# Optimization experiments

Hardware: AMD Instinct MI355X
Metric: run time of the kernel (lower is better)

## Reference

```python
import jax, jax.numpy as jnp
import numpy as np

# Asymmetric NF4 lookup table: NFQuantizer.create_normal_map(offset=0.9677083, num_bits=4)
NF4_TABLE = jnp.array([
    -1.0, -0.6961928009986877, -0.5250730514526367, -0.39491748809814453,
    -0.28444138169288635, -0.18477343022823334, -0.09105003625154495, 0.0,
    0.07958029955625534, 0.16093020141124725, 0.24611230194568634,
    0.33791524171829224, 0.44070982933044434, 0.5626170039176941,
    0.7229568362236023, 1.0], dtype=jnp.float32)

OUT_FEATURES = 4096
IN_FEATURES = 4096
BLOCK_SIZE = 64
NUM_BITS = 4

def setup_inputs() -> dict:
    key = jax.random.key(0)
    k1, k2, k3, k4, k5 = jax.random.split(key, 5)
    n_packed = OUT_FEATURES * IN_FEATURES // (8 // NUM_BITS)      # 8388608
    n_blocks = OUT_FEATURES * IN_FEATURES // BLOCK_SIZE            # 262144
    return {
        "input": jax.random.normal(k1, (2, 1024, IN_FEATURES), dtype=jnp.float32),
        "qweight": jax.random.randint(k2, (n_packed, 1), 0, 256, dtype=jnp.int32),
        "absmax": jax.random.uniform(k3, (n_blocks, 1), dtype=jnp.float32, minval=0.01, maxval=0.05),
        "lora_A": jax.random.normal(k4, (64, IN_FEATURES), dtype=jnp.float32) * 0.02,
        "lora_B": jax.random.normal(k5, (OUT_FEATURES, 64), dtype=jnp.float32) * 0.02,
    }

def dequantize_block(qweight, absmax):
    q = qweight[:, 0]                         # [N/2] packed bytes (int)
    low = NF4_TABLE[q & 0xF]                  # sub-code i=0 (low nibble first)
    high = NF4_TABLE[(q >> 4) & 0xF]          # sub-code i=1
    w = jnp.stack([low, high], axis=-1)       # [N/2, 2], matches torch column order
    w = w.reshape(-1, BLOCK_SIZE) * absmax    # per-block rescale, absmax [n_blocks,1]
    return w.reshape(OUT_FEATURES, IN_FEATURES)

def reference(input, qweight, absmax, lora_A, lora_B):
    weight = dequantize_block(qweight, absmax)          # [out, in] fp32
    ret = input @ weight.T                              # [B, S, out]
    lora = (input @ lora_A.T) @ lora_B.T                # low-rank path
    return ret + lora
```

## Files before the change

kernel.cpp:

```cpp
#include <hip/hip_runtime.h>
#include <hip/hip_bf16.h>
#include <stdint.h>

#define M_DIM 2048
#define N_DIM 4096
#define K_DIM 4096

typedef __attribute__((ext_vector_type(8))) __bf16 bf16x8;
typedef __attribute__((ext_vector_type(4))) float f32x4;
typedef __attribute__((ext_vector_type(8))) unsigned short u16x8;

__device__ __constant__ float NF4_TAB[16] = {
    -1.0f, -0.6961928009986877f, -0.5250730514526367f, -0.39491748809814453f,
    -0.28444138169288635f, -0.18477343022823334f, -0.09105003625154495f, 0.0f,
    0.07958029955625534f, 0.16093020141124725f, 0.24611230194568634f,
    0.33791524171829224f, 0.44070982933044434f, 0.5626170039176941f,
    0.7229568362236023f, 1.0f};

__device__ inline unsigned short f2b(float f) {
  union { float f; uint32_t u; } v; v.f = f;
  uint32_t u = v.u;
  return (unsigned short)((u + 0x7fffu + ((u >> 16) & 1u)) >> 16);
}

__global__ void k_cvt(const float4* __restrict__ in, ushort4* __restrict__ out, int n) {
  int i = blockIdx.x * 256 + threadIdx.x;
  if (i < n) {
    float4 v = in[i];
    ushort4 o;
    o.x = f2b(v.x); o.y = f2b(v.y); o.z = f2b(v.z); o.w = f2b(v.w);
    out[i] = o;
  }
}

__global__ void __launch_bounds__(256) k_build_w(const int* __restrict__ qw,
                                                 const float* __restrict__ am,
                                                 unsigned short* __restrict__ W) {
  __shared__ float tab[16];
  const int t = threadIdx.x;
  if (t < 16) tab[t] = NF4_TAB[t];
  __syncthreads();
  size_t i = (size_t)blockIdx.x * 256 + t;
  int4 q = *(const int4*)(qw + i * 4);
  float amv = am[i >> 3];
  u16x8 o;
  o[0] = f2b(tab[q.x & 15] * amv);  o[1] = f2b(tab[(q.x >> 4) & 15] * amv);
  o[2] = f2b(tab[q.y & 15] * amv);  o[3] = f2b(tab[(q.y >> 4) & 15] * amv);
  o[4] = f2b(tab[q.z & 15] * amv);  o[5] = f2b(tab[(q.z >> 4) & 15] * amv);
  o[6] = f2b(tab[q.w & 15] * amv);  o[7] = f2b(tab[(q.w >> 4) & 15] * amv);
  *(u16x8*)(W + i * 8) = o;
}

__global__ void __launch_bounds__(256) k_lora_u(const unsigned short* __restrict__ A16,
                                                const unsigned short* __restrict__ lA16,
                                                float* __restrict__ Up) {
  const int ln = threadIdx.x & 63, w = threadIdx.x >> 6;
  const int lr = ln & 15, lk = ln >> 4;
  const int mslab = blockIdx.x & 15;
  const int kc = blockIdx.x >> 4;
  const int m0 = mslab * 128 + w * 32;
  const int k0 = kc * 256;
  f32x4 acc[2][4] = {};
#pragma unroll
  for (int kk = 0; kk < 256; kk += 32) {
    bf16x8 af[2], bv[4];
#pragma unroll
    for (int mi = 0; mi < 2; ++mi)
      af[mi] = *(const bf16x8*)(A16 + (size_t)(m0 + mi * 16 + lr) * K_DIM + k0 + kk + lk * 8);
#pragma unroll
    for (int ni = 0; ni < 4; ++ni)
      bv[ni] = *(const bf16x8*)(lA16 + (size_t)(ni * 16 + lr) * K_DIM + k0 + kk + lk * 8);
#pragma unroll
    for (int mi = 0; mi < 2; ++mi)
#pragma unroll
      for (int ni = 0; ni < 4; ++ni)
        acc[mi][ni] = __builtin_amdgcn_mfma_f32_16x16x32_bf16(af[mi], bv[ni],
                                                              acc[mi][ni], 0, 0, 0);
  }
  float* up = Up + (size_t)kc * (M_DIM * 64);
#pragma unroll
  for (int mi = 0; mi < 2; ++mi)
#pragma unroll
    for (int ni = 0; ni < 4; ++ni)
#pragma unroll
      for (int r = 0; r < 4; ++r)
        up[(size_t)(m0 + mi * 16 + lk * 4 + r) * 64 + ni * 16 + lr] = acc[mi][ni][r];
}

__global__ void k_lora_red(const float4* __restrict__ Up, ushort4* __restrict__ U16) {
  int i = blockIdx.x * 256 + threadIdx.x;
  float4 s = Up[i];
#pragma unroll
  for (int c = 1; c < 16; ++c) {
    float4 p = Up[(size_t)c * (M_DIM * 64 / 4) + i];
    s.x += p.x; s.y += p.y; s.z += p.z; s.w += p.w;
  }
  ushort4 o; o.x = f2b(s.x); o.y = f2b(s.y); o.z = f2b(s.z); o.w = f2b(s.w);
  U16[i] = o;
}

#define LDSBUF 24576

#define FENCE() asm volatile("" ::: "memory")
#define BAR() do { FENCE(); __builtin_amdgcn_s_barrier(); FENCE(); } while (0)

#define COMPUTE_PHASE(KS, BC)                                                    \
  do {                                                                           \
    bf16x8 af[4], bv[4];                                                         \
    _Pragma("unroll") for (int mi = 0; mi < 4; ++mi) {                           \
      int row = wr * 64 + mi * 16 + lr;                                          \
      int slot = (((KS) << 2) | lk) ^ (row & 7);                                 \
      af[mi] = *(const bf16x8*)((BC) + row * 64 + slot * 8);                     \
    }                                                                            \
    _Pragma("unroll") for (int ni = 0; ni < 4; ++ni) {                           \
      int row = wc * 64 + ni * 16 + lr;                                          \
      int slot = (((KS) << 2) | lk) ^ (row & 7);                                 \
      bv[ni] = *(const bf16x8*)((BC) + 8192 + row * 64 + slot * 8);              \
    }                                                                            \
    __builtin_amdgcn_s_setprio(1);                                               \
    _Pragma("unroll") for (int mi = 0; mi < 4; ++mi)                             \
    _Pragma("unroll") for (int ni = 0; ni < 4; ++ni)                             \
      acc[mi][ni] = __builtin_amdgcn_mfma_f32_16x16x32_bf16(                     \
          af[mi], bv[ni], acc[mi][ni], 0, 0, 0);                                 \
    __builtin_amdgcn_s_setprio(0);                                               \
  } while (0)

__global__ void __launch_bounds__(512, 2) k_gemm(const unsigned short* __restrict__ A,
                                                 const unsigned short* __restrict__ B,
                                                 const unsigned short* __restrict__ U,
                                                 const unsigned short* __restrict__ LB,
                                                 float* __restrict__ C) {
  __shared__ unsigned short lds[3 * LDSBUF];
  const int tid = threadIdx.x;
  const int ln = tid & 63;
  const int wid = tid >> 6;
  const int wr = wid >> 2;
  const int wc = wid & 3;
  const int lr = ln & 15;
  const int lk = ln >> 4;

  const int sw = (blockIdx.x & 7) * 32 + (blockIdx.x >> 3);
  const int bm = sw & 15;
  const int bn = sw >> 4;
  const size_t arow0 = (size_t)bm * 128;
  const size_t brow0 = (size_t)bn * 256;

  const int srow = (wid << 3) + (ln >> 3);
  const int gs0 = (ln & 7) ^ (srow & 7);
  auto stage = [&](const unsigned short* __restrict__ G, size_t stride, size_t grow0,
                   int kt, unsigned short* dst) {
    const char* g = (const char*)(G + (grow0 + srow) * stride) + kt * 128 + gs0 * 16;
    __builtin_amdgcn_global_load_lds(
        (const __attribute__((address_space(1))) uint32_t*)g,
        (__attribute__((address_space(3))) uint32_t*)(dst + (size_t)(wid << 3) * 64),
        16, 0, 0);
  };

  f32x4 acc[4][4] = {};

  stage(A, K_DIM, arow0, 0, lds);
  stage(A, K_DIM, arow0 + 64, 0, lds + 4096);
  stage(B, K_DIM, brow0, 0, lds + 8192);
  stage(B, K_DIM, brow0 + 64, 0, lds + 12288);
  stage(B, K_DIM, brow0 + 128, 0, lds + 16384);
  stage(B, K_DIM, brow0 + 192, 0, lds + 20480);
  {
    unsigned short* b1 = lds + LDSBUF;
    stage(A, K_DIM, arow0, 1, b1);
    stage(A, K_DIM, arow0 + 64, 1, b1 + 4096);
    stage(B, K_DIM, brow0, 1, b1 + 8192);
    stage(B, K_DIM, brow0 + 64, 1, b1 + 12288);
    stage(B, K_DIM, brow0 + 128, 1, b1 + 16384);
    stage(B, K_DIM, brow0 + 192, 1, b1 + 20480);
  }
  asm volatile("s_waitcnt vmcnt(6)" ::: "memory");
  BAR();

  int cb = 0, sb = 2;
#pragma unroll 1
  for (int t = 0; t < 65; ++t) {
    const unsigned short* bc = lds + cb * LDSBUF;
    unsigned short* sd = lds + sb * LDSBUF;
    int kt2 = t + 2;
    const bool lora = (kt2 >= 64);
    const unsigned short* GA = lora ? U : A;
    const unsigned short* GB = lora ? LB : B;
    const size_t str = lora ? 64 : (size_t)K_DIM;
    const int ktv = lora ? 0 : kt2;

    stage(GA, str, arow0, ktv, sd);
    stage(GA, str, arow0 + 64, ktv, sd + 4096);
    stage(GB, str, brow0, ktv, sd + 8192);
    COMPUTE_PHASE(0, bc);
    BAR();

    stage(GB, str, brow0 + 64, ktv, sd + 12288);
    stage(GB, str, brow0 + 128, ktv, sd + 16384);
    stage(GB, str, brow0 + 192, ktv, sd + 20480);
    COMPUTE_PHASE(1, bc);
    asm volatile("s_waitcnt vmcnt(6)" ::: "memory");
    BAR();

    cb = (cb == 2) ? 0 : cb + 1;
    sb = (sb == 2) ? 0 : sb + 1;
  }

  float* Cb = C + (arow0 + (size_t)wr * 64) * N_DIM + brow0 + wc * 64;
#pragma unroll
  for (int mi = 0; mi < 4; ++mi)
#pragma unroll
    for (int ni = 0; ni < 4; ++ni)
#pragma unroll
      for (int r = 0; r < 4; ++r)
        Cb[(size_t)(mi * 16 + lk * 4 + r) * N_DIM + ni * 16 + lr] = acc[mi][ni][r];
}

extern "C" void kernel_launch(void* const* d_in, const int* in_sizes, int n_in,
                              void* d_out, int out_size, void* d_ws, size_t ws_size,
                              hipStream_t stream) {
  const float* input  = (const float*)d_in[0];
  const int* qweight  = (const int*)d_in[1];
  const float* absmax = (const float*)d_in[2];
  const float* lora_A = (const float*)d_in[3];
  const float* lora_B = (const float*)d_in[4];
  float* out = (float*)d_out;

  unsigned short* A16  = (unsigned short*)d_ws;
  unsigned short* B16  = A16 + (size_t)M_DIM * K_DIM;
  unsigned short* lB16 = B16 + (size_t)N_DIM * K_DIM;
  unsigned short* lA16 = lB16 + (size_t)N_DIM * 64;
  unsigned short* U16  = lA16 + (size_t)64 * K_DIM;
  float* Up = (float*)B16;

  k_cvt<<<(M_DIM * K_DIM / 4) / 256, 256, 0, stream>>>((const float4*)input,
                                                       (ushort4*)A16, M_DIM * K_DIM / 4);
  k_cvt<<<(64 * K_DIM / 4) / 256, 256, 0, stream>>>((const float4*)lora_A,
                                                    (ushort4*)lA16, 64 * K_DIM / 4);
  k_cvt<<<(N_DIM * 64 / 4) / 256, 256, 0, stream>>>((const float4*)lora_B,
                                                    (ushort4*)lB16, N_DIM * 64 / 4);
  k_lora_u<<<256, 256, 0, stream>>>(A16, lA16, Up);
  k_lora_red<<<(M_DIM * 64 / 4) / 256, 256, 0, stream>>>((const float4*)Up,
                                                         (ushort4*)U16);
  k_build_w<<<(N_DIM * K_DIM / 8) / 256, 256, 0, stream>>>(qweight, absmax, B16);
  k_gemm<<<256, 512, 0, stream>>>(A16, B16, U16, lB16, out);
}
```

Measured before the change: 108.0 us.

## Fuse bf16 conversion launches and restructure GEMM LDS-read/MFMA scheduling

Merges the three fp32-to-bf16 conversion kernels into one launch that dispatches on block index, removing two kernel launches. In the GEMM main loop, each half-step now issues its LDS fragment reads first, then the global stage loads, then a barrier, and only then the MFMA cluster. The MFMA cluster is fenced with lgkmcnt(0) and a sched_barrier, followed by an extra barrier. The intent is to overlap LDS reads with the global load issue and keep the MFMA cluster dense. The cost is two extra barriers per k-step, which may stall waves.

```diff
diff --git a/kernel.cpp b/kernel.cpp
--- a/kernel.cpp
+++ b/kernel.cpp
@@ -23,14 +23,20 @@
   return (unsigned short)((u + 0x7fffu + ((u >> 16) & 1u)) >> 16);
 }
 
-__global__ void k_cvt(const float4* __restrict__ in, ushort4* __restrict__ out, int n) {
-  int i = blockIdx.x * 256 + threadIdx.x;
-  if (i < n) {
-    float4 v = in[i];
-    ushort4 o;
-    o.x = f2b(v.x); o.y = f2b(v.y); o.z = f2b(v.z); o.w = f2b(v.w);
-    out[i] = o;
-  }
+__global__ void k_cvt3(const float4* __restrict__ in, ushort4* __restrict__ A16,
+                       const float4* __restrict__ lA, ushort4* __restrict__ lA16,
+                       const float4* __restrict__ lB, ushort4* __restrict__ lB16) {
+  int b = blockIdx.x;
+  const float4* src;
+  ushort4* dst;
+  int i;
+  if (b < 8192)      { src = in; dst = A16;  i = b * 256 + threadIdx.x; }
+  else if (b < 8448) { src = lA; dst = lA16; i = (b - 8192) * 256 + threadIdx.x; }
+  else               { src = lB; dst = lB16; i = (b - 8448) * 256 + threadIdx.x; }
+  float4 v = src[i];
+  ushort4 o;
+  o.x = f2b(v.x); o.y = f2b(v.y); o.z = f2b(v.z); o.w = f2b(v.w);
+  dst[i] = o;
 }
 
 __global__ void __launch_bounds__(256) k_build_w(const int* __restrict__ qw,
@@ -104,24 +110,27 @@
 #define FENCE() asm volatile("" ::: "memory")
 #define BAR() do { FENCE(); __builtin_amdgcn_s_barrier(); FENCE(); } while (0)
 
-#define COMPUTE_PHASE(KS, BC)                                                    \
+#define READ_FRAGS(KS, BC, AF, BV)                                               \
   do {                                                                           \
-    bf16x8 af[4], bv[4];                                                         \
     _Pragma("unroll") for (int mi = 0; mi < 4; ++mi) {                           \
       int row = wr * 64 + mi * 16 + lr;                                          \
       int slot = (((KS) << 2) | lk) ^ (row & 7);                                 \
-      af[mi] = *(const bf16x8*)((BC) + row * 64 + slot * 8);                     \
+      AF[mi] = *(const bf16x8*)((BC) + row * 64 + slot * 8);                     \
     }                                                                            \
     _Pragma("unroll") for (int ni = 0; ni < 4; ++ni) {                           \
       int row = wc * 64 + ni * 16 + lr;                                          \
       int slot = (((KS) << 2) | lk) ^ (row & 7);                                 \
-      bv[ni] = *(const bf16x8*)((BC) + 8192 + row * 64 + slot * 8);              \
+      BV[ni] = *(const bf16x8*)((BC) + 8192 + row * 64 + slot * 8);              \
     }                                                                            \
+  } while (0)
+
+#define MFMA_CLUSTER(AF, BV)                                                     \
+  do {                                                                           \
     __builtin_amdgcn_s_setprio(1);                                               \
     _Pragma("unroll") for (int mi = 0; mi < 4; ++mi)                             \
     _Pragma("unroll") for (int ni = 0; ni < 4; ++ni)                             \
       acc[mi][ni] = __builtin_amdgcn_mfma_f32_16x16x32_bf16(                     \
-          af[mi], bv[ni], acc[mi][ni], 0, 0, 0);                                 \
+          AF[mi], BV[ni], acc[mi][ni], 0, 0, 0);                                 \
     __builtin_amdgcn_s_setprio(0);                                               \
   } while (0)
 
@@ -188,18 +197,32 @@
     const size_t str = lora ? 64 : (size_t)K_DIM;
     const int ktv = lora ? 0 : kt2;
 
-    stage(GA, str, arow0, ktv, sd);
-    stage(GA, str, arow0 + 64, ktv, sd + 4096);
-    stage(GB, str, brow0, ktv, sd + 8192);
-    COMPUTE_PHASE(0, bc);
-    BAR();
-
-    stage(GB, str, brow0 + 64, ktv, sd + 12288);
-    stage(GB, str, brow0 + 128, ktv, sd + 16384);
-    stage(GB, str, brow0 + 192, ktv, sd + 20480);
-    COMPUTE_PHASE(1, bc);
-    asm volatile("s_waitcnt vmcnt(6)" ::: "memory");
-    BAR();
+    {
+      bf16x8 af[4], bv[4];
+      READ_FRAGS(0, bc, af, bv);
+      stage(GA, str, arow0, ktv, sd);
+      stage(GA, str, arow0 + 64, ktv, sd + 4096);
+      stage(GB, str, brow0, ktv, sd + 8192);
+      BAR();
+      asm volatile("s_waitcnt lgkmcnt(0)" ::: "memory");
+      __builtin_amdgcn_sched_barrier(0);
+      MFMA_CLUSTER(af, bv);
+      BAR();
+    }
+
+    {
+      bf16x8 af[4], bv[4];
+      READ_FRAGS(1, bc, af, bv);
+      stage(GB, str, brow0 + 64, ktv, sd + 12288);
+      stage(GB, str, brow0 + 128, ktv, sd + 16384);
+      stage(GB, str, brow0 + 192, ktv, sd + 20480);
+      asm volatile("s_waitcnt vmcnt(6)" ::: "memory");
+      BAR();
+      asm volatile("s_waitcnt lgkmcnt(0)" ::: "memory");
+      __builtin_amdgcn_sched_barrier(0);
+      MFMA_CLUSTER(af, bv);
+      BAR();
+    }
 
     cb = (cb == 2) ? 0 : cb + 1;
     sb = (sb == 2) ? 0 : sb + 1;
@@ -232,12 +255,9 @@
   unsigned short* U16  = lA16 + (size_t)64 * K_DIM;
   float* Up = (float*)B16;
 
-  k_cvt<<<(M_DIM * K_DIM / 4) / 256, 256, 0, stream>>>((const float4*)input,
-                                                       (ushort4*)A16, M_DIM * K_DIM / 4);
-  k_cvt<<<(64 * K_DIM / 4) / 256, 256, 0, stream>>>((const float4*)lora_A,
-                                                    (ushort4*)lA16, 64 * K_DIM / 4);
-  k_cvt<<<(N_DIM * 64 / 4) / 256, 256, 0, stream>>>((const float4*)lora_B,
-                                                    (ushort4*)lB16, N_DIM * 64 / 4);
+  k_cvt3<<<8704, 256, 0, stream>>>((const float4*)input, (ushort4*)A16,
+                                   (const float4*)lora_A, (ushort4*)lA16,
+                                   (const float4*)lora_B, (ushort4*)lB16);
   k_lora_u<<<256, 256, 0, stream>>>(A16, lA16, Up);
   k_lora_red<<<(M_DIM * 64 / 4) / 256, 256, 0, stream>>>((const float4*)Up,
                                                          (ushort4*)U16);
```

New measurement: 104.3 us. 1.04x faster.
